# Performance work log

Hardware: AMD Instinct MI355X
Metric: run time of the kernel (lower is better)

The kernel has to match this reference:

```python
import jax, jax.numpy as jnp
import numpy as np

B, T, D, H, O = 128, 512, 128, 256, 1


def setup_inputs() -> dict:
    key = jax.random.key(0)
    ks = jax.random.split(key, 11)
    s = lambda n: 1.0 / np.sqrt(H)
    u = lambda k, shape: jax.random.uniform(k, shape, jnp.float32, -s(0), s(0))
    return {
        "X": jax.random.normal(ks[0], (B, T, D), jnp.float32),
        "Wih0": u(ks[1], (4 * H, D)),
        "Whh0": u(ks[2], (4 * H, H)),
        "bih0": u(ks[3], (4 * H,)),
        "bhh0": u(ks[4], (4 * H,)),
        "Wih1": u(ks[5], (4 * H, H)),
        "Whh1": u(ks[6], (4 * H, H)),
        "bih1": u(ks[7], (4 * H,)),
        "bhh1": u(ks[8], (4 * H,)),
        "Wfc": u(ks[9], (O, H)),
        "bfc": u(ks[10], (O,)),
    }


def _lstm_layer(x, Wih, Whh, bih, bhh):
    # x: [B, T, Din] -> h sequence [B, T, H]
    # Precompute input contributions for all timesteps (one big GEMM).
    xg = jnp.einsum("btd,gd->btg", x, Wih) + bih + bhh  # [B, T, 4H]
    xg = jnp.transpose(xg, (1, 0, 2))  # [T, B, 4H]
    h0 = jnp.zeros((x.shape[0], Whh.shape[1]), x.dtype)
    c0 = jnp.zeros_like(h0)

    def step(carry, xt):
        h, c = carry
        gates = xt + h @ Whh.T  # [B, 4H]
        i, f, g, o = jnp.split(gates, 4, axis=-1)  # PyTorch gate order i,f,g,o
        i = jax.nn.sigmoid(i)
        f = jax.nn.sigmoid(f)
        g = jnp.tanh(g)
        o = jax.nn.sigmoid(o)
        c = f * c + i * g
        h = o * jnp.tanh(c)
        return (h, c), h

    (_, _), hs = jax.lax.scan(step, (h0, c0), xg)
    return jnp.transpose(hs, (1, 0, 2))  # [B, T, H]


def reference(X, Wih0, Whh0, bih0, bhh0, Wih1, Whh1, bih1, bhh1, Wfc, bfc):
    h1 = _lstm_layer(X, Wih0, Whh0, bih0, bhh0)
    h2 = _lstm_layer(h1, Wih1, Whh1, bih1, bhh1)
    return h2[:, -1, :] @ Wfc.T + bfc  # [B, O]
```

## Files before the change

### kernel.cpp

```cpp
#include <hip/hip_runtime.h>

typedef unsigned short u16;
typedef __attribute__((ext_vector_type(8))) short bf8;
typedef __attribute__((ext_vector_type(4))) float f4;

#define DEVI static __device__ __forceinline__

constexpr int Bb = 128, Tt = 512, Dd = 128, Hh = 256, G4 = 1024;
constexpr int CH  = 64;
constexpr int NCH = Tt / CH;
constexpr int MCH = CH * Bb;

DEVI u16 f2bf(float f) {
  union { float f; unsigned u; } v; v.f = f;
  unsigned r = v.u + 0x7FFFu + ((v.u >> 16) & 1u);
  return (u16)(r >> 16);
}
DEVI float bf2f(u16 b) { union { unsigned u; float f; } v; v.u = ((unsigned)b) << 16; return v.f; }
DEVI float frcp(float x) { return __builtin_amdgcn_rcpf(x); }
DEVI float sigm(float x) { return frcp(1.f + __expf(-x)); }
DEVI float tanh_f(float x) { return 1.f - 2.f * frcp(1.f + __expf(2.f * x)); }
DEVI f4 mfma16(bf8 a, bf8 b, f4 c) {
  return __builtin_amdgcn_mfma_f32_16x16x32_bf16(a, b, c, 0, 0, 0);
}
DEVI bf8 ld_coh16(const u16* p) {
  bf8 r;
  asm volatile("global_load_dwordx4 %0, %1, off sc0 sc1" : "=&v"(r) : "v"(p) : "memory");
  return r;
}
DEVI void st_coh16(u16* p, bf8 v) {
  asm volatile("global_store_dwordx4 %0, %1, off sc0 sc1" :: "v"(p), "v"(v) : "memory");
}
DEVI void st_coh4(unsigned* p, unsigned v) {
  asm volatile("global_store_dword %0, %1, off sc0 sc1" :: "v"(p), "v"(v) : "memory");
}


__global__ void k_prep_x(const float* __restrict__ X, u16* __restrict__ Xhi, u16* __restrict__ Xlo) {
  size_t idx = (size_t)blockIdx.x * 256 + threadIdx.x;
  int d = (int)(idx % Dd);
  size_t bt = idx / Dd;
  int b = (int)(bt / Tt), t = (int)(bt % Tt);
  float x = X[idx];
  u16 hi = f2bf(x);
  u16 lo = f2bf(x - bf2f(hi));
  size_t o = ((size_t)t * Bb + b) * Dd + d;
  Xhi[o] = hi; Xlo[o] = lo;
}

__global__ void k_split(const float* __restrict__ W, u16* __restrict__ hi_, u16* __restrict__ lo_) {
  size_t idx = (size_t)blockIdx.x * 256 + threadIdx.x;
  float v = W[idx];
  u16 hi = f2bf(v);
  hi_[idx] = hi;
  lo_[idx] = f2bf(v - bf2f(hi));
}

__global__ void k_prep_whh(const float* __restrict__ Whh, u16* __restrict__ W2) {
  int idx = blockIdx.x * 256 + threadIdx.x;
  int i = idx & 7, lane = (idx >> 3) & 63, kt = (idx >> 9) & 7, jtg = idx >> 12;
  int jp = (jtg << 4) + (lane & 15);
  int k  = ((lane >> 4) << 3) + i + (kt << 5);
  W2[idx] = f2bf(Whh[(size_t)jp * Hh + k]);
}

__global__ void k_bias(const float* __restrict__ a, const float* __restrict__ b, float* __restrict__ o) {
  int i = blockIdx.x * 256 + threadIdx.x;
  if (i < G4) o[i] = a[i] + b[i];
}

__global__ void k_init_tags(unsigned* __restrict__ tg) {
  int i = blockIdx.x * 256 + threadIdx.x;
  if (i < 2 * (Tt + 1) * 64) {
    int row = (i >> 6) % (Tt + 1);
    tg[i] = (row == 0) ? 1u : 0u;
  }
}

__global__ void k_zrow(u16* __restrict__ a, u16* __restrict__ b) {
  int i = blockIdx.x * 256 + threadIdx.x;
  if (i < Bb * Hh) { a[i] = 0; b[i] = 0; }
}

template <int K, bool ALO>
__global__ void __launch_bounds__(256) k_gemm(
    const u16* __restrict__ Ahi, const u16* __restrict__ Alo,
    const u16* __restrict__ Whi, const u16* __restrict__ Wlo,
    const float* __restrict__ bias, float* __restrict__ Cout) {
  __shared__ u16 AsH[128][32];
  __shared__ u16 AsL[128][32];
  const int tid = threadIdx.x, l = tid & 63;
  const int w = tid >> 6, wm = w >> 1, wn = w & 1;
  const int lrow = l & 15, lk = (l >> 4) << 3;
  const size_t m0 = (size_t)blockIdx.x * 128;
  const int n0 = blockIdx.y * 128;

  f4 acc[4][4];
  size_t colK[4];
#pragma unroll
  for (int ni = 0; ni < 4; ++ni) {
    int col = n0 + wn * 64 + ni * 16 + lrow;
    float bv = bias[col];
    colK[ni] = (size_t)col * K + lk;
#pragma unroll
    for (int mi = 0; mi < 4; ++mi) {
      acc[mi][ni][0] = bv; acc[mi][ni][1] = bv; acc[mi][ni][2] = bv; acc[mi][ni][3] = bv;
    }
  }

  for (int kk = 0; kk < K; kk += 32) {
    __syncthreads();
#pragma unroll
    for (int s = 0; s < 2; ++s) {
      int slot = s * 256 + tid;
      int r = slot >> 2, kg = (slot & 3) << 3;
      *(bf8*)&AsH[r][kg] = *(const bf8*)&Ahi[(m0 + r) * K + kk + kg];
      if constexpr (ALO) *(bf8*)&AsL[r][kg] = *(const bf8*)&Alo[(m0 + r) * K + kk + kg];
    }
    __syncthreads();

    bf8 bh[4], bl[4];
#pragma unroll
    for (int ni = 0; ni < 4; ++ni) {
      bh[ni] = *(const bf8*)&Whi[colK[ni] + kk];
      bl[ni] = *(const bf8*)&Wlo[colK[ni] + kk];
    }
    bf8 ah[4], al[4];
#pragma unroll
    for (int mi = 0; mi < 4; ++mi) {
      ah[mi] = *(const bf8*)&AsH[wm * 64 + mi * 16 + lrow][lk];
      if constexpr (ALO) al[mi] = *(const bf8*)&AsL[wm * 64 + mi * 16 + lrow][lk];
    }
#pragma unroll
    for (int mi = 0; mi < 4; ++mi)
#pragma unroll
      for (int ni = 0; ni < 4; ++ni) {
        acc[mi][ni] = mfma16(ah[mi], bh[ni], acc[mi][ni]);
        acc[mi][ni] = mfma16(ah[mi], bl[ni], acc[mi][ni]);
        if constexpr (ALO) acc[mi][ni] = mfma16(al[mi], bh[ni], acc[mi][ni]);
      }
  }

  f4* C4 = (f4*)Cout;
  const int by = blockIdx.y;
#pragma unroll
  for (int mi = 0; mi < 4; ++mi) {
    int gg = wm * 4 + mi;
#pragma unroll
    for (int ni = 0; ni < 4; ++ni) {
      int colb = by * 128 + wn * 64 + ni * 16;
      int q  = colb >> 8;
      int ss = (colb >> 5) & 7;
      int wt = (colb >> 4) & 1;
      C4[(((((size_t)blockIdx.x * 8 + gg) * 8 + ss) * 2 + wt) * 4 + q) * 64 + l] = acc[mi][ni];
    }
  }
}

__global__ void __launch_bounds__(128) k_recur(
    const float* __restrict__ xgA, const u16* __restrict__ WA,
    u16* __restrict__ hA, float* __restrict__ cA,
    const float* __restrict__ xgB, const u16* __restrict__ WB,
    u16* __restrict__ hB, float* __restrict__ cB,
    unsigned* __restrict__ tags,
    int t0A, int t0B, int actA, int actB) {
  __shared__ u16 wlds[32768];
  __shared__ u16 sbuf[512];
  const int role = blockIdx.x >> 6, sub = blockIdx.x & 63;
  if (role ? !actB : !actA) return;
  const float* xg = role ? xgB : xgA;
  const u16* W2 = role ? WB : WA;
  u16* h = role ? hB : hA;
  float* cst = role ? cB : cA;
  const int t0 = role ? t0B : t0A;
  unsigned* tg = tags + (size_t)role * (Tt + 1) * 64;

  const int tid = threadIdx.x, l = tid & 63, w = tid >> 6;
  const int lrow = l & 15, lg = l >> 4;
  const int g = sub & 7, s = sub >> 3;
  const int b_base = g << 4;
  const int jmy = (s << 5) + (w << 4) + lrow;

  for (int u = 0; u < 32; ++u) {
    int f = u * 128 + tid;
    int jl = f >> 9, kt = (f >> 6) & 7, e = f & 63;
    int jtg = ((jl >> 1) << 4) + (s << 1) + (jl & 1);
    *(bf8*)&wlds[f << 3] = *(const bf8*)&W2[((size_t)jtg << 12) + (kt << 9) + (e << 3)];
  }

  float cc4[4];
  if (t0 == 0) {
    cc4[0] = cc4[1] = cc4[2] = cc4[3] = 0.f;
  } else {
#pragma unroll
    for (int rr = 0; rr < 4; ++rr)
      cc4[rr] = cst[(size_t)(b_base + (lg << 2) + rr) * Hh + jmy];
  }
  __syncthreads();

  const f4* xb = (const f4*)xg + ((((size_t)g * 8 + s) * 2 + w) * 4) * 64 + l;
  f4 xgn[4];
#pragma unroll
  for (int q = 0; q < 4; ++q) xgn[q] = xb[q << 6];

  for (int t = 0; t < CH; ++t) {
    const int T = t0 + t;
    const unsigned tagv = (unsigned)(T + 1);

    f4 xg2[4];
    {
      int tn = (t + 1 < CH) ? t + 1 : t;
#pragma unroll
      for (int q = 0; q < 4; ++q) xg2[q] = xb[(size_t)tn * 32768 + (q << 6)];
    }

    unsigned* tgr = tg + (size_t)T * 64 + (g << 3);
    for (;;) {
      unsigned ok = 1;
#pragma unroll
      for (int p = 0; p < 8; ++p)
        ok &= (__hip_atomic_load(&tgr[p], __ATOMIC_RELAXED, __HIP_MEMORY_SCOPE_AGENT) == tagv);
      if (ok) break;
      __builtin_amdgcn_s_sleep(1);
    }
    __builtin_amdgcn_sched_barrier(0);

    const u16* hr = h + ((size_t)(role ? (T & 1) : T) * Bb + b_base + lrow) * Hh + (lg << 3);
    bf8 af[8];
#pragma unroll
    for (int kt = 0; kt < 8; ++kt) af[kt] = ld_coh16(hr + (kt << 5));

    f4 acc[4];
#pragma unroll
    for (int q = 0; q < 4; ++q) acc[q] = xgn[q];

#pragma unroll
    for (int kt = 0; kt < 8; ++kt) {
      bf8 bfr[4];
#pragma unroll
      for (int q = 0; q < 4; ++q)
        bfr[q] = *(const bf8*)&wlds[(((((q << 1) | w) << 3) | kt) << 9) + (l << 3)];
      asm volatile("s_waitcnt vmcnt(%0)" :: "i"(7 - kt) : "memory");
      __builtin_amdgcn_sched_barrier(0);
#pragma unroll
      for (int q = 0; q < 4; ++q) acc[q] = mfma16(af[kt], bfr[q], acc[q]);
    }

    u16 hv[4];
#pragma unroll
    for (int rr = 0; rr < 4; ++rr) {
      float gi = sigm(acc[0][rr]);
      float gf = sigm(acc[1][rr]);
      float gg = tanh_f(acc[2][rr]);
      float go = sigm(acc[3][rr]);
      float c2 = gf * cc4[rr] + gi * gg;
      cc4[rr] = c2;
      hv[rr] = f2bf(go * tanh_f(c2));
    }

#pragma unroll
    for (int rr = 0; rr < 4; ++rr)
      sbuf[(((lg << 2) + rr) << 5) + (w << 4) + lrow] = hv[rr];
    asm volatile("s_waitcnt lgkmcnt(0)\ns_barrier" ::: "memory");
    if (tid < 64) {
      int b = tid >> 2, gg = tid & 3;
      bf8 v = *(const bf8*)&sbuf[(b << 5) + (gg << 3)];
      u16* hw = h + ((size_t)(role ? ((T + 1) & 1) : (T + 1)) * Bb + b_base + b) * Hh
                + (s << 5) + (gg << 3);
      st_coh16(hw, v);
      asm volatile("s_waitcnt vmcnt(0)" ::: "memory");
      if (tid == 0)
        st_coh4(tg + (size_t)(T + 1) * 64 + (g << 3) + s, tagv + 1);
    }
#pragma unroll
    for (int q = 0; q < 4; ++q) xgn[q] = xg2[q];
  }

#pragma unroll
  for (int rr = 0; rr < 4; ++rr)
    cst[(size_t)(b_base + (lg << 2) + rr) * Hh + jmy] = cc4[rr];
}

__global__ void k_fc(const u16* __restrict__ h2l, const float* __restrict__ Wfc,
                     const float* __restrict__ bfc, float* __restrict__ out) {
  int b = threadIdx.x;
  if (b < Bb) {
    float s = bfc[0];
    for (int j = 0; j < Hh; ++j) s += bf2f(h2l[(size_t)b * Hh + j]) * Wfc[j];
    out[b] = s;
  }
}

extern "C" void kernel_launch(void* const* d_in, const int* in_sizes, int n_in,
                              void* d_out, int out_size, void* d_ws, size_t ws_size,
                              hipStream_t stream) {
  const float* X    = (const float*)d_in[0];
  const float* Wih0 = (const float*)d_in[1];
  const float* Whh0 = (const float*)d_in[2];
  const float* bih0 = (const float*)d_in[3];
  const float* bhh0 = (const float*)d_in[4];
  const float* Wih1 = (const float*)d_in[5];
  const float* Whh1 = (const float*)d_in[6];
  const float* bih1 = (const float*)d_in[7];
  const float* bhh1 = (const float*)d_in[8];
  const float* Wfc  = (const float*)d_in[9];
  const float* bfc  = (const float*)d_in[10];

  char* base = (char*)d_ws;
  size_t off = 0;
  auto alloc = [&](size_t bytes) -> char* {
    char* p = base + off;
    off = (off + bytes + 255) & ~(size_t)255;
    return p;
  };

  u16* Xhi = (u16*)alloc((size_t)Bb * Tt * Dd * 2);
  u16* Xlo = (u16*)alloc((size_t)Bb * Tt * Dd * 2);
  u16* W0h = (u16*)alloc((size_t)G4 * Dd * 2);
  u16* W0l = (u16*)alloc((size_t)G4 * Dd * 2);
  u16* W1h = (u16*)alloc((size_t)G4 * Hh * 2);
  u16* W1l = (u16*)alloc((size_t)G4 * Hh * 2);
  u16* W2a = (u16*)alloc((size_t)G4 * Hh * 2);
  u16* W2b = (u16*)alloc((size_t)G4 * Hh * 2);
  float* b0 = (float*)alloc(G4 * 4);
  float* b1 = (float*)alloc(G4 * 4);
  float* xgbA = (float*)alloc((size_t)MCH * G4 * 4);
  float* xgbB = (float*)alloc((size_t)MCH * G4 * 4);
  u16* h1Z = (u16*)alloc((size_t)(Tt + 1) * Bb * Hh * 2);
  u16* hB2 = (u16*)alloc((size_t)2 * Bb * Hh * 2);
  float* cstA = (float*)alloc((size_t)Bb * Hh * 4);
  float* cstB = (float*)alloc((size_t)Bb * Hh * 4);
  unsigned* tags = (unsigned*)alloc((size_t)2 * (Tt + 1) * 64 * 4);

  k_init_tags<<<(2 * (Tt + 1) * 64 + 255) / 256, 256, 0, stream>>>(tags);
  k_zrow<<<(Bb * Hh + 255) / 256, 256, 0, stream>>>(h1Z, hB2);
  k_prep_x<<<(Bb * Tt * Dd) / 256, 256, 0, stream>>>(X, Xhi, Xlo);
  k_split<<<(G4 * Dd) / 256, 256, 0, stream>>>(Wih0, W0h, W0l);
  k_split<<<(G4 * Hh) / 256, 256, 0, stream>>>(Wih1, W1h, W1l);
  k_prep_whh<<<(G4 * Hh) / 256, 256, 0, stream>>>(Whh0, W2a);
  k_prep_whh<<<(G4 * Hh) / 256, 256, 0, stream>>>(Whh1, W2b);
  k_bias<<<4, 256, 0, stream>>>(bih0, bhh0, b0);
  k_bias<<<4, 256, 0, stream>>>(bih1, bhh1, b1);

  for (int c = 0; c <= NCH; ++c) {
    if (c < NCH)
      k_gemm<Dd, true><<<dim3(CH, 8), 256, 0, stream>>>(
          Xhi + (size_t)c * MCH * Dd, Xlo + (size_t)c * MCH * Dd, W0h, W0l, b0, xgbA);
    if (c >= 1)
      k_gemm<Hh, false><<<dim3(CH, 8), 256, 0, stream>>>(
          h1Z + (size_t)((c - 1) * CH + 1) * Bb * Hh, nullptr, W1h, W1l, b1, xgbB);
    k_recur<<<128, 128, 0, stream>>>(xgbA, W2a, h1Z, cstA,
                                     xgbB, W2b, hB2, cstB, tags,
                                     c * CH, (c - 1) * CH,
                                     c < NCH ? 1 : 0, c >= 1 ? 1 : 0);
  }
  k_fc<<<1, 128, 0, stream>>>(hB2, Wfc, bfc, (float*)d_out);

  (void)in_sizes; (void)n_in; (void)out_size; (void)ws_size;
}
```

Measured before the change: 1.658 ms.

## Fuse input GEMMs and recurrence into one software-pipelined mega-kernel per chunk

Merges the layer-0 input GEMM, layer-1 input GEMM and both recurrence roles into a single launch per pipeline stage. Double-buffered xg arrays let the GEMM for the next chunk run alongside the recurrence for the current one. Chunk size drops from 64 to 32 steps. The recurrence now prefetches h speculatively before the tag wait, double-buffers the weight fragments read from LDS, and polls tags with a bounded spin. The intent is to remove serialization between the GEMM launches and the recurrence launches. In exchange the recurrence blocks now use 256 threads of which only 128 compute, the mega-kernel needs 66.5KB of LDS which lowers occupancy, and the shorter chunks mean more launches.

Result: faster. 1.551 ms (-6.4%).

```diff
diff --git a/kernel.cpp b/kernel.cpp
--- a/kernel.cpp
+++ b/kernel.cpp
@@ -1,37 +1,46 @@
 #include <hip/hip_runtime.h>
 
 typedef unsigned short u16;
+typedef unsigned int u32;
 typedef __attribute__((ext_vector_type(8))) short bf8;
 typedef __attribute__((ext_vector_type(4))) float f4;
 
 #define DEVI static __device__ __forceinline__
 
 constexpr int Bb = 128, Tt = 512, Dd = 128, Hh = 256, G4 = 1024;
-constexpr int CH  = 64;
+constexpr int CH  = 32;
 constexpr int NCH = Tt / CH;
 constexpr int MCH = CH * Bb;
+constexpr size_t CHF = (size_t)MCH * G4;
 
 DEVI u16 f2bf(float f) {
-  union { float f; unsigned u; } v; v.f = f;
-  unsigned r = v.u + 0x7FFFu + ((v.u >> 16) & 1u);
+  union { float f; u32 u; } v; v.f = f;
+  u32 r = v.u + 0x7FFFu + ((v.u >> 16) & 1u);
   return (u16)(r >> 16);
 }
-DEVI float bf2f(u16 b) { union { unsigned u; float f; } v; v.u = ((unsigned)b) << 16; return v.f; }
+DEVI float bf2f(u16 b) { union { u32 u; float f; } v; v.u = ((u32)b) << 16; return v.f; }
 DEVI float frcp(float x) { return __builtin_amdgcn_rcpf(x); }
 DEVI float sigm(float x) { return frcp(1.f + __expf(-x)); }
 DEVI float tanh_f(float x) { return 1.f - 2.f * frcp(1.f + __expf(2.f * x)); }
 DEVI f4 mfma16(bf8 a, bf8 b, f4 c) {
   return __builtin_amdgcn_mfma_f32_16x16x32_bf16(a, b, c, 0, 0, 0);
 }
-DEVI bf8 ld_coh16(const u16* p) {
+
+DEVI u32 ld_u32_coh(const u32* p) {
+  u32 r;
+  asm volatile("global_load_dword %0, %1, off sc0 sc1\ns_waitcnt vmcnt(0)"
+               : "=&v"(r) : "v"(p) : "memory");
+  return r;
+}
+DEVI bf8 ld16_coh(const u16* p) {
   bf8 r;
   asm volatile("global_load_dwordx4 %0, %1, off sc0 sc1" : "=&v"(r) : "v"(p) : "memory");
   return r;
 }
-DEVI void st_coh16(u16* p, bf8 v) {
+DEVI void st16_coh(u16* p, bf8 v) {
   asm volatile("global_store_dwordx4 %0, %1, off sc0 sc1" :: "v"(p), "v"(v) : "memory");
 }
-DEVI void st_coh4(unsigned* p, unsigned v) {
+DEVI void st_u32_coh(u32* p, u32 v) {
   asm volatile("global_store_dword %0, %1, off sc0 sc1" :: "v"(p), "v"(v) : "memory");
 }
 
@@ -69,11 +78,11 @@
   if (i < G4) o[i] = a[i] + b[i];
 }
 
-__global__ void k_init_tags(unsigned* __restrict__ tg) {
+__global__ void k_init(u32* __restrict__ tags) {
   int i = blockIdx.x * 256 + threadIdx.x;
   if (i < 2 * (Tt + 1) * 64) {
     int row = (i >> 6) % (Tt + 1);
-    tg[i] = (row == 0) ? 1u : 0u;
+    tags[i] = (row == 0) ? 1u : 0u;
   }
 }
 
@@ -83,17 +92,17 @@
 }
 
 template <int K, bool ALO>
-__global__ void __launch_bounds__(256) k_gemm(
-    const u16* __restrict__ Ahi, const u16* __restrict__ Alo,
-    const u16* __restrict__ Whi, const u16* __restrict__ Wlo,
-    const float* __restrict__ bias, float* __restrict__ Cout) {
-  __shared__ u16 AsH[128][32];
-  __shared__ u16 AsL[128][32];
+DEVI void gemm_body(char* smem, const u16* __restrict__ Ahi, const u16* __restrict__ Alo,
+                    const u16* __restrict__ Whi, const u16* __restrict__ Wlo,
+                    const float* __restrict__ bias, float* __restrict__ Cout,
+                    int bx, int by) {
+  u16* AsH = (u16*)smem;
+  u16* AsL = (u16*)(smem + 8192);
   const int tid = threadIdx.x, l = tid & 63;
   const int w = tid >> 6, wm = w >> 1, wn = w & 1;
   const int lrow = l & 15, lk = (l >> 4) << 3;
-  const size_t m0 = (size_t)blockIdx.x * 128;
-  const int n0 = blockIdx.y * 128;
+  const size_t m0 = (size_t)bx * 128;
+  const int n0 = by * 128;
 
   f4 acc[4][4];
   size_t colK[4];
@@ -114,8 +123,8 @@
     for (int s = 0; s < 2; ++s) {
       int slot = s * 256 + tid;
       int r = slot >> 2, kg = (slot & 3) << 3;
-      *(bf8*)&AsH[r][kg] = *(const bf8*)&Ahi[(m0 + r) * K + kk + kg];
-      if constexpr (ALO) *(bf8*)&AsL[r][kg] = *(const bf8*)&Alo[(m0 + r) * K + kk + kg];
+      *(bf8*)&AsH[r * 32 + kg] = *(const bf8*)&Ahi[(m0 + r) * K + kk + kg];
+      if constexpr (ALO) *(bf8*)&AsL[r * 32 + kg] = *(const bf8*)&Alo[(m0 + r) * K + kk + kg];
     }
     __syncthreads();
 
@@ -128,8 +137,8 @@
     bf8 ah[4], al[4];
 #pragma unroll
     for (int mi = 0; mi < 4; ++mi) {
-      ah[mi] = *(const bf8*)&AsH[wm * 64 + mi * 16 + lrow][lk];
-      if constexpr (ALO) al[mi] = *(const bf8*)&AsL[wm * 64 + mi * 16 + lrow][lk];
+      ah[mi] = *(const bf8*)&AsH[(wm * 64 + mi * 16 + lrow) * 32 + lk];
+      if constexpr (ALO) al[mi] = *(const bf8*)&AsL[(wm * 64 + mi * 16 + lrow) * 32 + lk];
     }
 #pragma unroll
     for (int mi = 0; mi < 4; ++mi)
@@ -142,7 +151,6 @@
   }
 
   f4* C4 = (f4*)Cout;
-  const int by = blockIdx.y;
 #pragma unroll
   for (int mi = 0; mi < 4; ++mi) {
     int gg = wm * 4 + mi;
@@ -152,133 +160,158 @@
       int q  = colb >> 8;
       int ss = (colb >> 5) & 7;
       int wt = (colb >> 4) & 1;
-      C4[(((((size_t)blockIdx.x * 8 + gg) * 8 + ss) * 2 + wt) * 4 + q) * 64 + l] = acc[mi][ni];
-    }
-  }
-}
-
-__global__ void __launch_bounds__(128) k_recur(
-    const float* __restrict__ xgA, const u16* __restrict__ WA,
-    u16* __restrict__ hA, float* __restrict__ cA,
-    const float* __restrict__ xgB, const u16* __restrict__ WB,
-    u16* __restrict__ hB, float* __restrict__ cB,
-    unsigned* __restrict__ tags,
-    int t0A, int t0B, int actA, int actB) {
-  __shared__ u16 wlds[32768];
-  __shared__ u16 sbuf[512];
-  const int role = blockIdx.x >> 6, sub = blockIdx.x & 63;
-  if (role ? !actB : !actA) return;
-  const float* xg = role ? xgB : xgA;
-  const u16* W2 = role ? WB : WA;
-  u16* h = role ? hB : hA;
-  float* cst = role ? cB : cA;
-  const int t0 = role ? t0B : t0A;
-  unsigned* tg = tags + (size_t)role * (Tt + 1) * 64;
-
+      C4[(((((size_t)bx * 8 + gg) * 8 + ss) * 2 + wt) * 4 + q) * 64 + l] = acc[mi][ni];
+    }
+  }
+}
+
+DEVI void recur_body(char* smem, const float* __restrict__ xg, const u16* __restrict__ W2,
+                     u16* h, float* cst, u32* tags,
+                     int t0, int role, int sub) {
+  u16* wlds = (u16*)smem;
+  u16* sbuf = (u16*)(smem + 65536);
   const int tid = threadIdx.x, l = tid & 63, w = tid >> 6;
   const int lrow = l & 15, lg = l >> 4;
   const int g = sub & 7, s = sub >> 3;
   const int b_base = g << 4;
-  const int jmy = (s << 5) + (w << 4) + lrow;
-
-  for (int u = 0; u < 32; ++u) {
-    int f = u * 128 + tid;
+  const int w1 = w & 1;
+
+  for (int u = 0; u < 16; ++u) {
+    int f = u * 256 + tid;
     int jl = f >> 9, kt = (f >> 6) & 7, e = f & 63;
     int jtg = ((jl >> 1) << 4) + (s << 1) + (jl & 1);
     *(bf8*)&wlds[f << 3] = *(const bf8*)&W2[((size_t)jtg << 12) + (kt << 9) + (e << 3)];
   }
 
-  float cc4[4];
-  if (t0 == 0) {
-    cc4[0] = cc4[1] = cc4[2] = cc4[3] = 0.f;
-  } else {
+  const int jmy = (s << 5) + (w1 << 4) + lrow;
+  float cc4[4] = {0.f, 0.f, 0.f, 0.f};
+  if (tid < 128 && t0 > 0) {
 #pragma unroll
     for (int rr = 0; rr < 4; ++rr)
       cc4[rr] = cst[(size_t)(b_base + (lg << 2) + rr) * Hh + jmy];
   }
   __syncthreads();
 
-  const f4* xb = (const f4*)xg + ((((size_t)g * 8 + s) * 2 + w) * 4) * 64 + l;
+  const f4* xb = (const f4*)xg + ((((size_t)g * 8 + s) * 2 + w1) * 4) * 64 + l;
   f4 xgn[4];
-#pragma unroll
-  for (int q = 0; q < 4; ++q) xgn[q] = xb[q << 6];
+  if (tid < 128) {
+#pragma unroll
+    for (int q = 0; q < 4; ++q) xgn[q] = xb[q << 6];
+  }
 
   for (int t = 0; t < CH; ++t) {
     const int T = t0 + t;
-    const unsigned tagv = (unsigned)(T + 1);
-
-    f4 xg2[4];
-    {
-      int tn = (t + 1 < CH) ? t + 1 : t;
-#pragma unroll
-      for (int q = 0; q < 4; ++q) xg2[q] = xb[(size_t)tn * 32768 + (q << 6)];
-    }
-
-    unsigned* tgr = tg + (size_t)T * 64 + (g << 3);
-    for (;;) {
-      unsigned ok = 1;
-#pragma unroll
-      for (int p = 0; p < 8; ++p)
-        ok &= (__hip_atomic_load(&tgr[p], __ATOMIC_RELAXED, __HIP_MEMORY_SCOPE_AGENT) == tagv);
-      if (ok) break;
-      __builtin_amdgcn_s_sleep(1);
-    }
-    __builtin_amdgcn_sched_barrier(0);
-
-    const u16* hr = h + ((size_t)(role ? (T & 1) : T) * Bb + b_base + lrow) * Hh + (lg << 3);
-    bf8 af[8];
-#pragma unroll
-    for (int kt = 0; kt < 8; ++kt) af[kt] = ld_coh16(hr + (kt << 5));
-
-    f4 acc[4];
-#pragma unroll
-    for (int q = 0; q < 4; ++q) acc[q] = xgn[q];
-
-#pragma unroll
-    for (int kt = 0; kt < 8; ++kt) {
-      bf8 bfr[4];
+    if (tid < 128) {
+      const u32 tagv = (u32)(T + 1);
+      u32* tp = tags + ((((size_t)role * (Tt + 1) + T) * 8 + g) << 3) + (tid & 7);
+      const u16* hr = h + ((size_t)(role ? (T & 1) : T) * Bb + b_base + lrow) * Hh + (lg << 3);
+
+      int seen = (ld_u32_coh(tp) == tagv);
+      bf8 af[8];
+#pragma unroll
+      for (int kt = 0; kt < 8; ++kt) af[kt] = ld16_coh(hr + (kt << 5));
+      if (!__all(seen)) {
+        int it = 0;
+        do { seen = (ld_u32_coh(tp) == tagv); } while (!__all(seen) && ++it < (1 << 20));
+#pragma unroll
+        for (int kt = 0; kt < 8; ++kt) af[kt] = ld16_coh(hr + (kt << 5));
+      }
+      __builtin_amdgcn_sched_barrier(0);
+
+      f4 acc[4];
+#pragma unroll
+      for (int q = 0; q < 4; ++q) acc[q] = xgn[q];
+
+      bf8 bcur[4], bnxt[4];
 #pragma unroll
       for (int q = 0; q < 4; ++q)
-        bfr[q] = *(const bf8*)&wlds[(((((q << 1) | w) << 3) | kt) << 9) + (l << 3)];
-      asm volatile("s_waitcnt vmcnt(%0)" :: "i"(7 - kt) : "memory");
-      __builtin_amdgcn_sched_barrier(0);
-#pragma unroll
-      for (int q = 0; q < 4; ++q) acc[q] = mfma16(af[kt], bfr[q], acc[q]);
-    }
-
-    u16 hv[4];
-#pragma unroll
-    for (int rr = 0; rr < 4; ++rr) {
-      float gi = sigm(acc[0][rr]);
-      float gf = sigm(acc[1][rr]);
-      float gg = tanh_f(acc[2][rr]);
-      float go = sigm(acc[3][rr]);
-      float c2 = gf * cc4[rr] + gi * gg;
-      cc4[rr] = c2;
-      hv[rr] = f2bf(go * tanh_f(c2));
-    }
-
-#pragma unroll
-    for (int rr = 0; rr < 4; ++rr)
-      sbuf[(((lg << 2) + rr) << 5) + (w << 4) + lrow] = hv[rr];
-    asm volatile("s_waitcnt lgkmcnt(0)\ns_barrier" ::: "memory");
+        bcur[q] = *(const bf8*)&wlds[((((q << 1) | w1) << 3) << 9) + (l << 3)];
+#pragma unroll
+      for (int kt = 0; kt < 8; ++kt) {
+        if (kt < 7) {
+#pragma unroll
+          for (int q = 0; q < 4; ++q)
+            bnxt[q] = *(const bf8*)&wlds[(((((q << 1) | w1) << 3) | (kt + 1)) << 9) + (l << 3)];
+        }
+        asm volatile("s_waitcnt vmcnt(%0)" :: "i"(7 - kt) : "memory");
+        __builtin_amdgcn_sched_barrier(0);
+#pragma unroll
+        for (int q = 0; q < 4; ++q) acc[q] = mfma16(af[kt], bcur[q], acc[q]);
+#pragma unroll
+        for (int q = 0; q < 4; ++q) bcur[q] = bnxt[q];
+      }
+
+      u16 hv[4];
+#pragma unroll
+      for (int rr = 0; rr < 4; ++rr) {
+        float gi = sigm(acc[0][rr]);
+        float gf = sigm(acc[1][rr]);
+        float gg = tanh_f(acc[2][rr]);
+        float go = sigm(acc[3][rr]);
+        float c2 = gf * cc4[rr] + gi * gg;
+        cc4[rr] = c2;
+        hv[rr] = f2bf(go * tanh_f(c2));
+      }
+#pragma unroll
+      for (int rr = 0; rr < 4; ++rr)
+        sbuf[(((lg << 2) + rr) << 5) + (w1 << 4) + lrow] = hv[rr];
+    }
+    __syncthreads();
     if (tid < 64) {
       int b = tid >> 2, gg = tid & 3;
       bf8 v = *(const bf8*)&sbuf[(b << 5) + (gg << 3)];
       u16* hw = h + ((size_t)(role ? ((T + 1) & 1) : (T + 1)) * Bb + b_base + b) * Hh
                 + (s << 5) + (gg << 3);
-      st_coh16(hw, v);
+      st16_coh(hw, v);
       asm volatile("s_waitcnt vmcnt(0)" ::: "memory");
-      if (tid == 0)
-        st_coh4(tg + (size_t)(T + 1) * 64 + (g << 3) + s, tagv + 1);
-    }
-#pragma unroll
-    for (int q = 0; q < 4; ++q) xgn[q] = xg2[q];
-  }
-
-#pragma unroll
-  for (int rr = 0; rr < 4; ++rr)
-    cst[(size_t)(b_base + (lg << 2) + rr) * Hh + jmy] = cc4[rr];
+      if (tid == 0) {
+        u32* tq = tags + ((((size_t)role * (Tt + 1) + T + 1) * 8 + g) << 3) + s;
+        st_u32_coh(tq, (u32)(T + 2));
+      }
+    }
+    if (tid < 128 && t + 1 < CH) {
+#pragma unroll
+      for (int q = 0; q < 4; ++q) xgn[q] = xb[(size_t)(t + 1) * 32768 + (q << 6)];
+    }
+  }
+
+  if (tid < 128) {
+#pragma unroll
+    for (int rr = 0; rr < 4; ++rr)
+      cst[(size_t)(b_base + (lg << 2) + rr) * Hh + jmy] = cc4[rr];
+  }
+}
+
+__global__ void __launch_bounds__(256) k_mega(
+    const u16* gAh, const u16* gAl,
+    const u16* W0h, const u16* W0l, const float* b0,
+    const u16* gBa,
+    const u16* W1h, const u16* W1l, const float* b1,
+    float* xgAw, const float* xgAr,
+    float* xgBw, const float* xgBr,
+    const u16* W2a, const u16* W2b,
+    u16* h1, u16* h2r, float* cstA, float* cstB,
+    u32* tags, int d) {
+  __shared__ __align__(16) char smem[66560];
+  const int bid = blockIdx.x;
+  if (bid < 128) {
+    const int role = bid >> 6;
+    if (role == 0) {
+      if (d < 1 || d > NCH) return;
+      recur_body(smem, xgAr, W2a, h1, cstA, tags, (d - 1) * CH, 0, bid & 63);
+    } else {
+      if (d < 3 || d > NCH + 2) return;
+      recur_body(smem, xgBr, W2b, h2r, cstB, tags, (d - 3) * CH, 1, bid & 63);
+    }
+  } else if (bid < 384) {
+    if (d > NCH - 1) return;
+    int q = bid - 128;
+    gemm_body<Dd, true>(smem, gAh, gAl, W0h, W0l, b0, xgAw, q & 31, q >> 5);
+  } else {
+    if (d < 2 || d > NCH + 1) return;
+    int q = bid - 384;
+    gemm_body<Hh, false>(smem, gBa, nullptr, W1h, W1l, b1, xgBw, q & 31, q >> 5);
+  }
 }
 
 __global__ void k_fc(const u16* __restrict__ h2l, const float* __restrict__ Wfc,
@@ -324,16 +357,16 @@
   u16* W2b = (u16*)alloc((size_t)G4 * Hh * 2);
   float* b0 = (float*)alloc(G4 * 4);
   float* b1 = (float*)alloc(G4 * 4);
-  float* xgbA = (float*)alloc((size_t)MCH * G4 * 4);
-  float* xgbB = (float*)alloc((size_t)MCH * G4 * 4);
+  float* xgA = (float*)alloc((size_t)2 * CHF * 4);
+  float* xgB = (float*)alloc((size_t)2 * CHF * 4);
   u16* h1Z = (u16*)alloc((size_t)(Tt + 1) * Bb * Hh * 2);
-  u16* hB2 = (u16*)alloc((size_t)2 * Bb * Hh * 2);
+  u16* h2r = (u16*)alloc((size_t)2 * Bb * Hh * 2);
   float* cstA = (float*)alloc((size_t)Bb * Hh * 4);
   float* cstB = (float*)alloc((size_t)Bb * Hh * 4);
-  unsigned* tags = (unsigned*)alloc((size_t)2 * (Tt + 1) * 64 * 4);
-
-  k_init_tags<<<(2 * (Tt + 1) * 64 + 255) / 256, 256, 0, stream>>>(tags);
-  k_zrow<<<(Bb * Hh + 255) / 256, 256, 0, stream>>>(h1Z, hB2);
+  u32* tags = (u32*)alloc((size_t)2 * (Tt + 1) * 64 * 4);
+
+  k_init<<<(2 * (Tt + 1) * 64 + 255) / 256, 256, 0, stream>>>(tags);
+  k_zrow<<<(Bb * Hh + 255) / 256, 256, 0, stream>>>(h1Z, h2r);
   k_prep_x<<<(Bb * Tt * Dd) / 256, 256, 0, stream>>>(X, Xhi, Xlo);
   k_split<<<(G4 * Dd) / 256, 256, 0, stream>>>(Wih0, W0h, W0l);
   k_split<<<(G4 * Hh) / 256, 256, 0, stream>>>(Wih1, W1h, W1l);
@@ -342,19 +375,19 @@
   k_bias<<<4, 256, 0, stream>>>(bih0, bhh0, b0);
   k_bias<<<4, 256, 0, stream>>>(bih1, bhh1, b1);
 
-  for (int c = 0; c <= NCH; ++c) {
-    if (c < NCH)
-      k_gemm<Dd, true><<<dim3(CH, 8), 256, 0, stream>>>(
-          Xhi + (size_t)c * MCH * Dd, Xlo + (size_t)c * MCH * Dd, W0h, W0l, b0, xgbA);
-    if (c >= 1)
-      k_gemm<Hh, false><<<dim3(CH, 8), 256, 0, stream>>>(
-          h1Z + (size_t)((c - 1) * CH + 1) * Bb * Hh, nullptr, W1h, W1l, b1, xgbB);
-    k_recur<<<128, 128, 0, stream>>>(xgbA, W2a, h1Z, cstA,
-                                     xgbB, W2b, hB2, cstB, tags,
-                                     c * CH, (c - 1) * CH,
-                                     c < NCH ? 1 : 0, c >= 1 ? 1 : 0);
-  }
-  k_fc<<<1, 128, 0, stream>>>(hB2, Wfc, bfc, (float*)d_out);
+  for (int dd = 0; dd <= NCH + 2; ++dd) {
+    int ca = dd < NCH ? dd : NCH - 1;
+    int cb = dd < 2 ? 0 : (dd - 2 < NCH ? dd - 2 : NCH - 1);
+    k_mega<<<640, 256, 0, stream>>>(
+        Xhi + (size_t)ca * MCH * Dd, Xlo + (size_t)ca * MCH * Dd,
+        W0h, W0l, b0,
+        h1Z + ((size_t)(cb * CH) + 1) * Bb * Hh,
+        W1h, W1l, b1,
+        xgA + (size_t)(dd & 1) * CHF, xgA + (size_t)((dd + 1) & 1) * CHF,
+        xgB + (size_t)(dd & 1) * CHF, xgB + (size_t)((dd + 1) & 1) * CHF,
+        W2a, W2b, h1Z, h2r, cstA, cstB, tags, dd);
+  }
+  k_fc<<<1, 128, 0, stream>>>(h2r, Wfc, bfc, (float*)d_out);
 
   (void)in_sizes; (void)n_in; (void)out_size; (void)ws_size;
 }
```
